# Kernel optimization log

Hardware: AMD Instinct MI355X
Metric: run time of the kernel (lower is better)

The kernel has to match this reference:

```python
import jax, jax.numpy as jnp
import numpy as np
import math

N = 100000; NFEAT = 500; M = 512; HIDDEN = 128; NLAYER = 2; K = 10; NCLASS = 40; ALPHA = 0.1


def setup_inputs() -> dict:
    key = jax.random.key(0)
    ks = jax.random.split(key, 20)
    s_in = 1.0 / math.sqrt(NFEAT); s_h = 1.0 / math.sqrt(HIDDEN); s_e = 1.0 / math.sqrt(HIDDEN + 1)
    kvec = jnp.arange(K + 1, dtype=jnp.float32)
    fW = ALPHA * (1.0 - ALPHA) ** kvec
    fW = fW.at[-1].set((1.0 - ALPHA) ** K)
    return {
        "x": jax.random.normal(ks[0], (N, NFEAT), jnp.float32),
        "e0": jax.random.uniform(ks[1], (M,), jnp.float32) * 2.0,
        "e1": jax.random.uniform(ks[2], (M,), jnp.float32) * 2.0,
        "u0": jax.random.normal(ks[3], (N, M), jnp.float32) / math.sqrt(N),
        "u1": jax.random.normal(ks[4], (N, M), jnp.float32) / math.sqrt(N),
        "fe_w1": jax.random.uniform(ks[5], (NFEAT, HIDDEN), jnp.float32, -s_in, s_in),
        "fe_b1": jnp.zeros((HIDDEN,), jnp.float32),
        "fe_w2": jax.random.uniform(ks[6], (HIDDEN, HIDDEN), jnp.float32, -s_h, s_h),
        "fe_b2": jnp.zeros((HIDDEN,), jnp.float32),
        "eig_w": jax.random.uniform(ks[7], (HIDDEN + 1, 1), jnp.float32, -s_e, s_e),
        "eig_b": jnp.zeros((1,), jnp.float32),
        "layer_weight": 0.01 * jax.random.normal(ks[8], (NLAYER, 2, HIDDEN), jnp.float32),
        "ln_gamma": jnp.ones((NLAYER, HIDDEN), jnp.float32),
        "ln_beta": jnp.zeros((NLAYER, HIDDEN), jnp.float32),
        "fW": fW,
        "att0": jax.random.uniform(ks[9], (HIDDEN, 1), jnp.float32, -1.0, 1.0),
        "att1": jax.random.uniform(ks[10], (HIDDEN, 1), jnp.float32, -1.0, 1.0),
        "att2": jax.random.uniform(ks[11], (HIDDEN, 1), jnp.float32, -1.0, 1.0),
        "att_vec": jax.random.uniform(ks[12], (3, 3), jnp.float32, -1.0 / math.sqrt(3.0), 1.0 / math.sqrt(3.0)),
        "lin3_w": jax.random.uniform(ks[13], (HIDDEN, NCLASS), jnp.float32, -s_h, s_h),
        "lin3_b": jnp.zeros((NCLASS,), jnp.float32),
    }


def _fourier_encode(e, eig_w, eig_b):
    # e: [m] -> [m, 1]; constant-1 column then cos(k*pi*e), k=1..HIDDEN
    freqs = jnp.arange(1, HIDDEN + 1, dtype=e.dtype)
    eeig = jnp.concatenate([jnp.ones((e.shape[0], 1), e.dtype),
                            jnp.cos(math.pi * e[:, None] * freqs)], axis=1)
    return eeig @ eig_w + eig_b  # [m, 1]


def _mfnn_layer(feats, w, g, b):
    # feats: [N, 2, H]; weight [2, H] -> sum over bases, LayerNorm, ReLU
    h = jnp.sum(feats * w, axis=1)
    mu = jnp.mean(h, axis=-1, keepdims=True)
    var = jnp.var(h, axis=-1, keepdims=True)
    h = (h - mu) * jax.lax.rsqrt(var + 1e-5) * g + b
    return jax.nn.relu(h)


def reference(x, e0, e1, u0, u1, fe_w1, fe_b1, fe_w2, fe_b2, eig_w, eig_b,
              layer_weight, ln_gamma, ln_beta, fW, att0, att1, att2, att_vec,
              lin3_w, lin3_b):
    h = jax.nn.relu(x @ fe_w1 + fe_b1) @ fe_w2 + fe_b2  # feat_encoder (dropouts are eval no-ops)
    result = [h]
    tail = jnp.sum(fW[1:])  # r is invariant across the K inner steps: hidden = fW[0]*h + sum(fW[1:])*r
    for e_i, u_i in ((e0, u0), (e1, u1)):
        eig = _fourier_encode(e_i, eig_w, eig_b)  # [m, 1]
        for L in range(NLAYER):
            utx = u_i.T @ h                # [m, H]
            r = u_i @ (eig * utx)          # [N, H] spectral propagation
            hidden = h * fW[0] + tail * r
            feats = jnp.stack([h, hidden], axis=1)  # [N, 2, H]
            h = _mfnn_layer(feats, layer_weight[L], ln_gamma[L], ln_beta[L])
        result.append(h)
    logits = jax.nn.sigmoid(jnp.concatenate(
        [result[0] @ att0, result[1] @ att1, result[2] @ att2], axis=1)) @ att_vec
    att = jax.nn.softmax(logits, axis=1)  # [N, 3]
    h = att[:, 0:1] * result[0] + att[:, 1:2] * result[1] + att[:, 2:3] * result[2]
    return jax.nn.log_softmax(h @ lin3_w + lin3_b, axis=1)
```

## Files before the change

kernel.cpp:

```cpp
#include <hip/hip_runtime.h>
#include <stdint.h>

#define NR 100000L
#define KC 92
#define CHN 1088L

typedef __attribute__((ext_vector_type(8))) short s16x8;
typedef __attribute__((ext_vector_type(4))) short s16x4;
typedef __attribute__((ext_vector_type(4))) float f32x4;

__device__ __forceinline__ unsigned short f2bf(float f) {
  union { float f; unsigned u; } v; v.f = f;
  unsigned r = v.u + 0x7FFFu + ((v.u >> 16) & 1u);
  return (unsigned short)(r >> 16);
}
__device__ __forceinline__ float bf2f(unsigned short s) {
  union { unsigned u; float f; } v; v.u = ((unsigned)s) << 16;
  return v.f;
}
__device__ __forceinline__ f32x4 MF(s16x8 a, s16x8 b, f32x4 c) {
  return __builtin_amdgcn_mfma_f32_16x16x32_bf16(a, b, c, 0, 0, 0);
}


__device__ __forceinline__ int swz(int row, int col) {
  return row * 64 + (((col >> 3) ^ (row & 7)) << 3) + (col & 7);
}

__device__ __forceinline__ void gld16(const void* g, void* l) {
  __builtin_amdgcn_global_load_lds(
      (const __attribute__((address_space(1))) void*)g,
      (__attribute__((address_space(3))) void*)l, 16, 0, 0);
}

template<int ROWS>
__device__ __forceinline__ void stage_async(unsigned short* lds, const unsigned short* src,
    long pitch, long r0, long k0, int tid) {
  const int lane = tid & 63, w = tid >> 6;
  const int lr = lane >> 3, lc = lane & 7;
#pragma unroll
  for (int it = 0; it < ROWS / 32; ++it) {
    const int rowbase = w * (ROWS / 4) + it * 8;
    const int row = rowbase + lr;
    const int sc = lc ^ (row & 7);
    gld16(src + (r0 + row) * pitch + k0 + sc * 8, lds + rowbase * 64);
  }
}

template<int ROWS>
__device__ __forceinline__ void stage_guard(unsigned short* lds, const unsigned short* src,
    long pitch, long r0, long rlim, long k0, long klim, int tid) {
  const int f8 = tid & 7;
#pragma unroll
  for (int it = 0; it < ROWS / 32; ++it) {
    const int row = (tid >> 3) + it * 32;
    const long gr = r0 + row, gk = k0 + f8 * 8;
    s16x8 v = {};
    if (gr < rlim && gk < klim) v = *(const s16x8*)(src + gr * pitch + gk);
    *(s16x8*)(lds + row * 64 + ((f8 ^ (row & 7)) << 3)) = v;
  }
}

template<int ROWS>
__device__ __forceinline__ void stage_guard_f32(unsigned short* lds, const float* src,
    long pitch, long r0, long rlim, long k0, long klim, int tid) {
  const int f4 = tid & 15;
#pragma unroll
  for (int it = 0; it < ROWS / 16; ++it) {
    const int row = (tid >> 4) + it * 16;
    const long gr = r0 + row, gk = k0 + f4 * 4;
    f32x4 v = {};
    if (gr < rlim && gk < klim) v = *(const f32x4*)(src + gr * pitch + gk);
    s16x4 o;
    o[0] = (short)f2bf(v[0]); o[1] = (short)f2bf(v[1]);
    o[2] = (short)f2bf(v[2]); o[3] = (short)f2bf(v[3]);
    const int c = f4 >> 1, h = f4 & 1;
    *(s16x4*)(lds + row * 64 + ((c ^ (row & 7)) << 3) + h * 4) = o;
  }
}

__device__ __forceinline__ void stage_utr_f32(unsigned short* lds, const float* u,
    long n0, long m0, int tid) {
  const int mm = tid & 63;
  const int base = tid >> 6;
#pragma unroll
  for (int it = 0; it < 16; ++it) {
    const int nl = base + it * 4;
    const long n = n0 + nl;
    unsigned short v = 0;
    if (n < NR) v = f2bf(u[n * 512 + m0 + mm]);
    lds[swz(mm, nl)] = v;
  }
}

__device__ __forceinline__ s16x8 fragA(const unsigned short* lds, int row, int kk, int lane) {
  const int c = kk * 4 + (lane >> 4);
  return *(const s16x8*)(lds + row * 64 + ((c ^ (row & 7)) << 3));
}

__global__ void k_prep(const float* __restrict__ e0, const float* __restrict__ e1,
    const float* __restrict__ fe_w1, const float* __restrict__ fe_w2,
    const float* __restrict__ eig_w, const float* __restrict__ eig_b,
    const float* __restrict__ lw, const float* __restrict__ fW,
    unsigned short* __restrict__ W1T, unsigned short* __restrict__ W2T,
    float* __restrict__ eig, float* __restrict__ coef) {
  long id = (long)blockIdx.x * 256 + threadIdx.x;
  if (id < 65536) {
    int j = (int)(id >> 9), k = (int)(id & 511);
    W1T[id] = (k < 500) ? f2bf(fe_w1[(long)k * 128 + j]) : (unsigned short)0;
  } else if (id < 65536 + 16384) {
    long q = id - 65536; int j = (int)(q >> 7), k = (int)(q & 127);
    W2T[q] = f2bf(fe_w2[(long)k * 128 + j]);
  } else if (id < 65536 + 16384 + 1024) {
    long q = id - 65536 - 16384; int b = (int)(q >> 9), m = (int)(q & 511);
    const float* e = b ? e1 : e0;
    float s = eig_b[0] + eig_w[0];
    float pe = 3.14159265358979323846f * e[m];
    for (int f = 1; f <= 128; ++f) s += cosf(pe * (float)f) * eig_w[f];
    eig[q] = s;
  } else if (id < 65536 + 16384 + 1024 + 256) {
    long q = id - 65536 - 16384 - 1024; int L = (int)(q >> 7), j = (int)(q & 127);
    float tail = 0.f;
    for (int k = 1; k <= 10; ++k) tail += fW[k];
    float w0 = lw[L * 256 + j], w1 = lw[L * 256 + 128 + j];
    coef[L * 256 + j] = w0 + fW[0] * w1;
    coef[L * 256 + 128 + j] = tail * w1;
  }
}

__global__ __launch_bounds__(256) void k_cvtx(const float* __restrict__ x,
    unsigned short* __restrict__ xb) {
  const long t = (long)blockIdx.x * 256 + threadIdx.x;
  const int k4 = (int)(t & 127) * 4;
  const long n = t >> 7;
  s16x4 o = {};
  if (k4 < 500) {
    f32x4 v = *(const f32x4*)(x + n * 500 + k4);
    o[0] = (short)f2bf(v[0]); o[1] = (short)f2bf(v[1]);
    o[2] = (short)f2bf(v[2]); o[3] = (short)f2bf(v[3]);
  }
  *(s16x4*)(xb + n * 512 + k4) = o;
}

__global__ __launch_bounds__(256) void k_cvtT(const float* __restrict__ u,
    unsigned short* __restrict__ Ubf, unsigned short* __restrict__ UbT) {
  __shared__ float T[64][68];
  const int tid = threadIdx.x;
  const int nt = blockIdx.x >> 3, mt = blockIdx.x & 7;
  const long n0 = (long)nt * 64, m0 = (long)mt * 64;
  const int c8 = (tid & 7) * 8;
  const int r = tid >> 3;
#pragma unroll
  for (int p = 0; p < 2; ++p) {
    const int rr = r + p * 32;
    const long n = n0 + rr;
    f32x4 a = {}, b = {};
    if (n < NR) {
      a = *(const f32x4*)(u + n * 512 + m0 + c8);
      b = *(const f32x4*)(u + n * 512 + m0 + c8 + 4);
    }
    *(f32x4*)&T[rr][c8] = a;
    *(f32x4*)&T[rr][c8 + 4] = b;
    if (n < NR) {
      s16x8 o;
      o[0] = (short)f2bf(a[0]); o[1] = (short)f2bf(a[1]);
      o[2] = (short)f2bf(a[2]); o[3] = (short)f2bf(a[3]);
      o[4] = (short)f2bf(b[0]); o[5] = (short)f2bf(b[1]);
      o[6] = (short)f2bf(b[2]); o[7] = (short)f2bf(b[3]);
      *(s16x8*)(Ubf + n * 512 + m0 + c8) = o;
    }
  }
  __syncthreads();
  const int nb8 = (tid & 7) * 8;
#pragma unroll
  for (int p = 0; p < 2; ++p) {
    const int mm = r + p * 32;
    s16x8 o;
#pragma unroll
    for (int e = 0; e < 8; ++e) o[e] = (short)f2bf(T[nb8 + e][mm]);
    const long nb = n0 + nb8;
    if (nb + 7 < NR) {
      *(s16x8*)(UbT + (long)(m0 + mm) * NR + nb) = o;
    } else {
#pragma unroll
      for (int e = 0; e < 8; ++e)
        if (nb + e < NR) UbT[(long)(m0 + mm) * NR + nb + e] = o[e];
    }
  }
}

__global__ __launch_bounds__(256) void k_gemm1(const unsigned short* __restrict__ xb,
    const unsigned short* __restrict__ W1T, const float* __restrict__ b1,
    unsigned short* __restrict__ t) {
  __shared__ __align__(16) unsigned short Al[128 * 64];
  __shared__ __align__(16) unsigned short Bl[128 * 64];
  const int tid = threadIdx.x, lane = tid & 63, w = tid >> 6;
  const long n0 = (long)blockIdx.x * 128;
  const bool edge = (n0 + 128) > NR;
  f32x4 acc[2][8] = {};
  for (int kt = 0; kt < 8; ++kt) {
    if (!edge) stage_async<128>(Al, xb, 512, n0, kt * 64L, tid);
    else       stage_guard<128>(Al, xb, 512, n0, NR, kt * 64L, 512, tid);
    stage_async<128>(Bl, W1T, 512, 0, kt * 64L, tid);
    __syncthreads();
#pragma unroll
    for (int kk = 0; kk < 2; ++kk) {
      s16x8 af0 = fragA(Al, w * 32 + (lane & 15), kk, lane);
      s16x8 af1 = fragA(Al, w * 32 + 16 + (lane & 15), kk, lane);
#pragma unroll
      for (int ct = 0; ct < 8; ++ct) {
        s16x8 bfr = fragA(Bl, ct * 16 + (lane & 15), kk, lane);
        acc[0][ct] = MF(af0, bfr, acc[0][ct]);
        acc[1][ct] = MF(af1, bfr, acc[1][ct]);
      }
    }
    __syncthreads();
  }
  const int cl = lane & 15, g = lane >> 4;
#pragma unroll
  for (int ct = 0; ct < 8; ++ct) {
    const int j = ct * 16 + cl;
    const float bias = b1[j];
#pragma unroll
    for (int rt = 0; rt < 2; ++rt)
#pragma unroll
      for (int r = 0; r < 4; ++r) {
        const long n = n0 + w * 32 + rt * 16 + (g << 2) + r;
        if (n < NR) {
          float v = acc[rt][ct][r] + bias;
          t[n * 128 + j] = f2bf(v > 0.f ? v : 0.f);
        }
      }
  }
}

__global__ __launch_bounds__(256) void k_gemm1f(const float* __restrict__ x,
    const unsigned short* __restrict__ W1T, const float* __restrict__ b1,
    unsigned short* __restrict__ t) {
  __shared__ __align__(16) unsigned short Al[64 * 64];
  __shared__ __align__(16) unsigned short Bl[128 * 64];
  const int tid = threadIdx.x, lane = tid & 63, w = tid >> 6;
  const long n0 = (long)blockIdx.x * 64;
  f32x4 acc[8] = {};
  for (int kt = 0; kt < 8; ++kt) {
    stage_guard_f32<64>(Al, x, 500, n0, NR, kt * 64L, 500, tid);
    stage_guard<128>(Bl, W1T, 512, 0, 1L << 40, kt * 64L, 512, tid);
    __syncthreads();
#pragma unroll
    for (int kk = 0; kk < 2; ++kk) {
      s16x8 af = fragA(Al, (w << 4) + (lane & 15), kk, lane);
#pragma unroll
      for (int ct = 0; ct < 8; ++ct) {
        s16x8 bfr = fragA(Bl, (ct << 4) + (lane & 15), kk, lane);
        acc[ct] = MF(af, bfr, acc[ct]);
      }
    }
    __syncthreads();
  }
  const int cl = lane & 15, g = lane >> 4;
#pragma unroll
  for (int ct = 0; ct < 8; ++ct) {
    int j = (ct << 4) + cl;
    float bias = b1[j];
#pragma unroll
    for (int r = 0; r < 4; ++r) {
      long n = n0 + (w << 4) + (g << 2) + r;
      if (n < NR) {
        float v = acc[ct][r] + bias;
        t[n * 128 + j] = f2bf(v > 0.f ? v : 0.f);
      }
    }
  }
}

__global__ __launch_bounds__(256) void k_gemm2(const unsigned short* __restrict__ W2T,
    const unsigned short* __restrict__ t, const float* __restrict__ b2,
    unsigned short* __restrict__ hT) {
  __shared__ __align__(16) unsigned short Al[128 * 64];
  __shared__ __align__(16) unsigned short Bl[128 * 64];
  const int tid = threadIdx.x, lane = tid & 63, w = tid >> 6;
  const long n0 = (long)blockIdx.x * 128;
  const bool edge = (n0 + 128) > NR;
  f32x4 acc[8][2] = {};
  for (int kt = 0; kt < 2; ++kt) {
    stage_async<128>(Al, W2T, 128, 0, kt * 64L, tid);
    if (!edge) stage_async<128>(Bl, t, 128, n0, kt * 64L, tid);
    else       stage_guard<128>(Bl, t, 128, n0, NR, kt * 64L, 128, tid);
    __syncthreads();
#pragma unroll
    for (int kk = 0; kk < 2; ++kk) {
      s16x8 bf0 = fragA(Bl, w * 32 + (lane & 15), kk, lane);
      s16x8 bf1 = fragA(Bl, w * 32 + 16 + (lane & 15), kk, lane);
#pragma unroll
      for (int rt = 0; rt < 8; ++rt) {
        s16x8 af = fragA(Al, rt * 16 + (lane & 15), kk, lane);
        acc[rt][0] = MF(af, bf0, acc[rt][0]);
        acc[rt][1] = MF(af, bf1, acc[rt][1]);
      }
    }
    __syncthreads();
  }
  const int cl = lane & 15, g = lane >> 4;
#pragma unroll
  for (int rt = 0; rt < 8; ++rt)
#pragma unroll
    for (int r = 0; r < 4; ++r) {
      const int j = rt * 16 + (g << 2) + r;
      const float bias = b2[j];
#pragma unroll
      for (int ct = 0; ct < 2; ++ct) {
        const long n = n0 + w * 32 + ct * 16 + cl;
        if (n < NR) hT[(long)j * NR + n] = f2bf(acc[rt][ct][r] + bias);
      }
    }
}

__global__ __launch_bounds__(256) void k_utx(const unsigned short* __restrict__ hT,
    const unsigned short* __restrict__ UbT, float* __restrict__ P) {
  __shared__ __align__(16) unsigned short Al[128 * 64];
  __shared__ __align__(16) unsigned short Bl[128 * 64];
  const int tid = threadIdx.x, lane = tid & 63, w = tid >> 6;
  const int mt = blockIdx.x & 3, c = blockIdx.x >> 2;
  const long m0 = (long)mt * 128, nb = (long)c * CHN;
  f32x4 acc[8][2] = {};
  for (int kt = 0; kt < 17; ++kt) {
    const long n0 = nb + kt * 64;
    if (n0 + 64 <= NR) {
      stage_async<128>(Al, hT, NR, 0, n0, tid);
      stage_async<128>(Bl, UbT, NR, m0, n0, tid);
    } else {
      stage_guard<128>(Al, hT, NR, 0, 1L << 40, n0, NR, tid);
      stage_guard<128>(Bl, UbT, NR, m0, 1L << 40, n0, NR, tid);
    }
    __syncthreads();
#pragma unroll
    for (int kk = 0; kk < 2; ++kk) {
      s16x8 bf0 = fragA(Bl, w * 32 + (lane & 15), kk, lane);
      s16x8 bf1 = fragA(Bl, w * 32 + 16 + (lane & 15), kk, lane);
#pragma unroll
      for (int rt = 0; rt < 8; ++rt) {
        s16x8 af = fragA(Al, rt * 16 + (lane & 15), kk, lane);
        acc[rt][0] = MF(af, bf0, acc[rt][0]);
        acc[rt][1] = MF(af, bf1, acc[rt][1]);
      }
    }
    __syncthreads();
  }
  const int cl = lane & 15, g = lane >> 4;
  float* Pc = P + (long)c * 65536;
#pragma unroll
  for (int rt = 0; rt < 8; ++rt)
#pragma unroll
    for (int r = 0; r < 4; ++r) {
      const int j = rt * 16 + (g << 2) + r;
#pragma unroll
      for (int ct = 0; ct < 2; ++ct) {
        const long m = m0 + w * 32 + ct * 16 + cl;
        Pc[(long)j * 512 + m] = acc[rt][ct][r];
      }
    }
}

__global__ __launch_bounds__(256) void k_utx0(const unsigned short* __restrict__ hT,
    const float* __restrict__ u, float* __restrict__ P) {
  __shared__ __align__(16) unsigned short Al[128 * 64];
  __shared__ __align__(16) unsigned short Bl[64 * 64];
  const int tid = threadIdx.x, lane = tid & 63, w = tid >> 6;
  const int mt = blockIdx.x & 7, c = blockIdx.x >> 3;
  const long m0 = (long)mt * 64, nb = (long)c * CHN;
  f32x4 acc[8] = {};
  for (int kt = 0; kt < 17; ++kt) {
    const long n0 = nb + kt * 64;
    stage_guard<128>(Al, hT, NR, 0, 1L << 40, n0, NR, tid);
    stage_utr_f32(Bl, u, n0, m0, tid);
    __syncthreads();
#pragma unroll
    for (int kk = 0; kk < 2; ++kk) {
      s16x8 bfr = fragA(Bl, (w << 4) + (lane & 15), kk, lane);
#pragma unroll
      for (int rt = 0; rt < 8; ++rt) {
        s16x8 af = fragA(Al, (rt << 4) + (lane & 15), kk, lane);
        acc[rt] = MF(af, bfr, acc[rt]);
      }
    }
    __syncthreads();
  }
  const int cl = lane & 15, g = lane >> 4;
  const long m = m0 + (w << 4) + cl;
  float* Pc = P + (long)c * 65536;
#pragma unroll
  for (int rt = 0; rt < 8; ++rt)
#pragma unroll
    for (int r = 0; r < 4; ++r) {
      int j = (rt << 4) + (g << 2) + r;
      Pc[(long)j * 512 + m] = acc[rt][r];
    }
}

__global__ void k_reduce(const float* __restrict__ P, const float* __restrict__ eig,
                         unsigned short* __restrict__ sT) {
  const int idx = blockIdx.x * 256 + threadIdx.x;
  const int m = idx & 511;
  float s = 0.f;
#pragma unroll 4
  for (int c = 0; c < KC; ++c) s += P[(long)c * 65536 + idx];
  sT[idx] = f2bf(s * eig[m]);
}

__global__ __launch_bounds__(256) void k_rgemm(const unsigned short* __restrict__ sT,
    const unsigned short* __restrict__ Ubf, const unsigned short* __restrict__ hin,
    unsigned short* __restrict__ hout, const float* __restrict__ c0,
    const float* __restrict__ c1, const float* __restrict__ gam,
    const float* __restrict__ bet) {
  __shared__ __align__(16) unsigned short Al[128 * 64];
  __shared__ __align__(16) unsigned short Bl[64 * 64];
  const int tid = threadIdx.x, lane = tid & 63, w = tid >> 6;
  const long n0 = (long)blockIdx.x * 64;
  const bool edge = (n0 + 64) > NR;
  f32x4 acc[8] = {};
  for (int kt = 0; kt < 8; ++kt) {
    stage_async<128>(Al, sT, 512, 0, kt * 64L, tid);
    if (!edge) stage_async<64>(Bl, Ubf, 512, n0, kt * 64L, tid);
    else       stage_guard<64>(Bl, Ubf, 512, n0, NR, kt * 64L, 512, tid);
    __syncthreads();
#pragma unroll
    for (int kk = 0; kk < 2; ++kk) {
      s16x8 bfr = fragA(Bl, (w << 4) + (lane & 15), kk, lane);
#pragma unroll
      for (int rt = 0; rt < 8; ++rt) {
        s16x8 af = fragA(Al, rt * 16 + (lane & 15), kk, lane);
        acc[rt] = MF(af, bfr, acc[rt]);
      }
    }
    __syncthreads();
  }
  if (!edge) stage_async<128>(Al, hin, NR, 0, n0, tid);
  else       stage_guard<128>(Al, hin, NR, 0, 1L << 40, n0, NR, tid);
  __syncthreads();
  const int cl = lane & 15, g = lane >> 4;
  const int nl = (w << 4) + cl;
  float sum = 0.f, ssq = 0.f;
#pragma unroll
  for (int rt = 0; rt < 8; ++rt)
#pragma unroll
    for (int r = 0; r < 4; ++r) {
      const int j = rt * 16 + (g << 2) + r;
      const float hp = bf2f(Al[swz(j, nl)]);
      const float pv = hp * c0[j] + c1[j] * acc[rt][r];
      acc[rt][r] = pv;
      sum += pv; ssq += pv * pv;
    }
  sum += __shfl_xor(sum, 16, 64); sum += __shfl_xor(sum, 32, 64);
  ssq += __shfl_xor(ssq, 16, 64); ssq += __shfl_xor(ssq, 32, 64);
  const float mu = sum * (1.f / 128.f);
  const float rs = rsqrtf(ssq * (1.f / 128.f) - mu * mu + 1e-5f);
  __syncthreads();
#pragma unroll
  for (int rt = 0; rt < 8; ++rt)
#pragma unroll
    for (int r = 0; r < 4; ++r) {
      const int j = rt * 16 + (g << 2) + r;
      float o = (acc[rt][r] - mu) * rs * gam[j] + bet[j];
      Al[swz(j, nl)] = f2bf(o > 0.f ? o : 0.f);
    }
  __syncthreads();
  const int f8 = tid & 7;
  const long gk = n0 + f8 * 8;
#pragma unroll
  for (int it = 0; it < 4; ++it) {
    const int j = (tid >> 3) + it * 32;
    const s16x8 v = *(const s16x8*)(Al + j * 64 + ((f8 ^ (j & 7)) << 3));
    if (gk + 7 < NR) {
      *(s16x8*)(hout + (long)j * NR + gk) = v;
    } else {
#pragma unroll
      for (int e = 0; e < 8; ++e)
        if (gk + e < NR) hout[(long)j * NR + gk + e] = v[e];
    }
  }
}

__global__ __launch_bounds__(256) void k_rgemm64(const unsigned short* __restrict__ sT,
    const float* __restrict__ u, const unsigned short* __restrict__ hin,
    unsigned short* __restrict__ hout, const float* __restrict__ c0,
    const float* __restrict__ c1, const float* __restrict__ gam,
    const float* __restrict__ bet) {
  __shared__ __align__(16) unsigned short Al[128 * 64];
  __shared__ __align__(16) unsigned short Bl[64 * 64];
  const int tid = threadIdx.x, lane = tid & 63, w = tid >> 6;
  const long n0 = (long)blockIdx.x * 64;
  f32x4 acc[8] = {};
  for (int kt = 0; kt < 8; ++kt) {
    stage_guard<128>(Al, sT, 512, 0, 1L << 40, kt * 64L, 512, tid);
    stage_guard_f32<64>(Bl, u, 512, n0, NR, kt * 64L, 512, tid);
    __syncthreads();
#pragma unroll
    for (int kk = 0; kk < 2; ++kk) {
      s16x8 bfr = fragA(Bl, (w << 4) + (lane & 15), kk, lane);
#pragma unroll
      for (int rt = 0; rt < 8; ++rt) {
        s16x8 af = fragA(Al, (rt << 4) + (lane & 15), kk, lane);
        acc[rt] = MF(af, bfr, acc[rt]);
      }
    }
    __syncthreads();
  }
  const int cl = lane & 15, g = lane >> 4;
  const long n = n0 + (w << 4) + cl;
  const bool valid = n < NR;
  float sum = 0.f, ssq = 0.f;
#pragma unroll
  for (int rt = 0; rt < 8; ++rt)
#pragma unroll
    for (int r = 0; r < 4; ++r) {
      int j = (rt << 4) + (g << 2) + r;
      float hp = valid ? bf2f(hin[(long)j * NR + n]) : 0.f;
      float pv = hp * c0[j] + c1[j] * acc[rt][r];
      acc[rt][r] = pv;
      sum += pv; ssq += pv * pv;
    }
  sum += __shfl_xor(sum, 16, 64); sum += __shfl_xor(sum, 32, 64);
  ssq += __shfl_xor(ssq, 16, 64); ssq += __shfl_xor(ssq, 32, 64);
  const float mu = sum * (1.f / 128.f);
  const float rs = rsqrtf(ssq * (1.f / 128.f) - mu * mu + 1e-5f);
  if (valid) {
#pragma unroll
    for (int rt = 0; rt < 8; ++rt)
#pragma unroll
      for (int r = 0; r < 4; ++r) {
        int j = (rt << 4) + (g << 2) + r;
        float o = (acc[rt][r] - mu) * rs * gam[j] + bet[j];
        hout[(long)j * NR + n] = f2bf(o > 0.f ? o : 0.f);
      }
  }
}

__global__ __launch_bounds__(256) void k_final(const unsigned short* __restrict__ R0,
    const unsigned short* __restrict__ R1, const unsigned short* __restrict__ R2,
    const float* __restrict__ att0, const float* __restrict__ att1,
    const float* __restrict__ att2, const float* __restrict__ av,
    const float* __restrict__ W, const float* __restrict__ bias,
    float* __restrict__ out) {
  __shared__ __align__(16) float Wl[128 * 40];
  __shared__ float Av[3][128];
  __shared__ float zb[256 * 41];
  const int tid = threadIdx.x;
  for (int i = tid; i < 5120; i += 256) Wl[i] = W[i];
  if (tid < 128) { Av[0][tid] = att0[tid]; Av[1][tid] = att1[tid]; Av[2][tid] = att2[tid]; }
  __syncthreads();
  const long n0 = (long)blockIdx.x * 256;
  const long n = n0 + tid;
  const long nn = n < NR ? n : NR - 1;
  float a0 = 0.f, a1 = 0.f, a2 = 0.f;
  for (int j = 0; j < 128; ++j) {
    a0 += bf2f(R0[(long)j * NR + nn]) * Av[0][j];
    a1 += bf2f(R1[(long)j * NR + nn]) * Av[1][j];
    a2 += bf2f(R2[(long)j * NR + nn]) * Av[2][j];
  }
  const float s0 = 1.f / (1.f + expf(-a0));
  const float s1 = 1.f / (1.f + expf(-a1));
  const float s2 = 1.f / (1.f + expf(-a2));
  const float l0 = s0 * av[0] + s1 * av[3] + s2 * av[6];
  const float l1 = s0 * av[1] + s1 * av[4] + s2 * av[7];
  const float l2 = s0 * av[2] + s1 * av[5] + s2 * av[8];
  const float mx = fmaxf(l0, fmaxf(l1, l2));
  const float e0v = expf(l0 - mx), e1v = expf(l1 - mx), e2v = expf(l2 - mx);
  const float inv = 1.f / (e0v + e1v + e2v);
  const float w0 = e0v * inv, w1 = e1v * inv, w2 = e2v * inv;
  float z[40];
#pragma unroll
  for (int c = 0; c < 40; ++c) z[c] = bias[c];
  for (int j = 0; j < 128; ++j) {
    const float h = w0 * bf2f(R0[(long)j * NR + nn]) + w1 * bf2f(R1[(long)j * NR + nn])
                  + w2 * bf2f(R2[(long)j * NR + nn]);
#pragma unroll
    for (int c4 = 0; c4 < 10; ++c4) {
      f32x4 wv = *(const f32x4*)(&Wl[j * 40 + c4 * 4]);
      z[c4 * 4 + 0] += h * wv[0];
      z[c4 * 4 + 1] += h * wv[1];
      z[c4 * 4 + 2] += h * wv[2];
      z[c4 * 4 + 3] += h * wv[3];
    }
  }
  float mz = z[0];
#pragma unroll
  for (int c = 1; c < 40; ++c) mz = fmaxf(mz, z[c]);
  float se = 0.f;
#pragma unroll
  for (int c = 0; c < 40; ++c) se += expf(z[c] - mz);
  const float ls = logf(se);
#pragma unroll
  for (int c = 0; c < 40; ++c) zb[tid * 41 + c] = z[c] - mz - ls;
  __syncthreads();
  long rows = NR - n0; if (rows > 256) rows = 256;
  const long cnt = rows * 40;
  for (long i = tid; i < cnt; i += 256)
    out[n0 * 40 + i] = zb[(i / 40) * 41 + (i % 40)];
}

extern "C" void kernel_launch(void* const* d_in, const int* in_sizes, int n_in,
                              void* d_out, int out_size, void* d_ws, size_t ws_size,
                              hipStream_t stream) {
  const float* x      = (const float*)d_in[0];
  const float* e0     = (const float*)d_in[1];
  const float* e1     = (const float*)d_in[2];
  const float* u0     = (const float*)d_in[3];
  const float* u1     = (const float*)d_in[4];
  const float* fe_w1  = (const float*)d_in[5];
  const float* fe_b1  = (const float*)d_in[6];
  const float* fe_w2  = (const float*)d_in[7];
  const float* fe_b2  = (const float*)d_in[8];
  const float* eig_w  = (const float*)d_in[9];
  const float* eig_bi = (const float*)d_in[10];
  const float* lw     = (const float*)d_in[11];
  const float* ln_g   = (const float*)d_in[12];
  const float* ln_b   = (const float*)d_in[13];
  const float* fW     = (const float*)d_in[14];
  const float* att0   = (const float*)d_in[15];
  const float* att1   = (const float*)d_in[16];
  const float* att2   = (const float*)d_in[17];
  const float* attv   = (const float*)d_in[18];
  const float* lin3w  = (const float*)d_in[19];
  const float* lin3b  = (const float*)d_in[20];
  float* out = (float*)d_out;

  const size_t SZ_H = (size_t)NR * 128 * 2;
  const size_t SZ_P = (size_t)KC * 65536 * 4;
  const size_t SZ_U = (size_t)NR * 512 * 2;
  const size_t SZ_X = (size_t)NR * 512 * 2;

  char* p = (char*)d_ws;
  unsigned short* R0T = (unsigned short*)p; p += SZ_H;
  unsigned short* R1T = (unsigned short*)p; p += SZ_H;
  unsigned short* R2T = (unsigned short*)p; p += SZ_H;
  float* P            = (float*)p;          p += SZ_P;
  unsigned short* W1T = (unsigned short*)p; p += 131072;
  unsigned short* W2T = (unsigned short*)p; p += 32768;
  unsigned short* sT  = (unsigned short*)p; p += 131072;
  float* eig          = (float*)p;          p += 4096;
  float* coef         = (float*)p;          p += 2048;
  const size_t base = (size_t)(p - (char*)d_ws);
  const bool full = ws_size >= base + SZ_X + 2 * SZ_U;
  unsigned short* xb  = nullptr;
  unsigned short* UbT = nullptr;
  unsigned short* Ubf = nullptr;
  if (full) {
    xb  = (unsigned short*)p; p += SZ_X;
    UbT = (unsigned short*)p; p += SZ_U;
    Ubf = (unsigned short*)p; p += SZ_U;
  }

  k_prep<<<325, 256, 0, stream>>>(e0, e1, fe_w1, fe_w2, eig_w, eig_bi, lw, fW,
                                  W1T, W2T, eig, coef);
  const int GB64  = (int)((NR + 63) / 64);
  const int GB128 = (int)((NR + 127) / 128);

  if (full) {
    k_cvtx<<<50000, 256, 0, stream>>>(x, xb);
    k_gemm1<<<GB128, 256, 0, stream>>>(xb, W1T, fe_b1, R1T);
  } else {
    k_gemm1f<<<GB64, 256, 0, stream>>>(x, W1T, fe_b1, R1T);
  }
  k_gemm2<<<GB128, 256, 0, stream>>>(W2T, R1T, fe_b2, R0T);

  for (int b = 0; b < 2; ++b) {
    const float* u = b ? u1 : u0;
    if (full) k_cvtT<<<GB64 * 8, 256, 0, stream>>>(u, Ubf, UbT);
    const unsigned short* hin = (b == 0) ? R0T : R1T;
    unsigned short* hb = b ? R2T : R1T;
    for (int L = 0; L < 2; ++L) {
      unsigned short* hout = hb;
      if (full) k_utx<<<4 * KC, 256, 0, stream>>>(hin, UbT, P);
      else      k_utx0<<<8 * KC, 256, 0, stream>>>(hin, u, P);
      k_reduce<<<256, 256, 0, stream>>>(P, eig + b * 512, sT);
      if (full)
        k_rgemm<<<GB64, 256, 0, stream>>>(sT, Ubf, hin, hout,
            coef + L * 256, coef + L * 256 + 128, ln_g + L * 128, ln_b + L * 128);
      else
        k_rgemm64<<<GB64, 256, 0, stream>>>(sT, u, hin, hout,
            coef + L * 256, coef + L * 256 + 128, ln_g + L * 128, ln_b + L * 128);
      hin = hout;
    }
  }
  k_final<<<(int)((NR + 255) / 256), 256, 0, stream>>>(R0T, R1T, R2T,
      att0, att1, att2, attv, lin3w, lin3b, out);
}
```

Measured before the change: 728.3 us.

## Double-buffer LDS staging in utx and rgemm kernels, split utx M tile

```diff
diff --git a/kernel.cpp b/kernel.cpp
--- a/kernel.cpp
+++ b/kernel.cpp
@@ -21,7 +21,6 @@
 __device__ __forceinline__ f32x4 MF(s16x8 a, s16x8 b, f32x4 c) {
   return __builtin_amdgcn_mfma_f32_16x16x32_bf16(a, b, c, 0, 0, 0);
 }
-
 
 __device__ __forceinline__ int swz(int row, int col) {
   return row * 64 + (((col >> 3) ^ (row & 7)) << 3) + (col & 7);
@@ -317,47 +316,58 @@
 
 __global__ __launch_bounds__(256) void k_utx(const unsigned short* __restrict__ hT,
     const unsigned short* __restrict__ UbT, float* __restrict__ P) {
-  __shared__ __align__(16) unsigned short Al[128 * 64];
-  __shared__ __align__(16) unsigned short Bl[128 * 64];
+  __shared__ __align__(16) unsigned short Al[2][128 * 64];
+  __shared__ __align__(16) unsigned short Bl[2][64 * 64];
   const int tid = threadIdx.x, lane = tid & 63, w = tid >> 6;
-  const int mt = blockIdx.x & 3, c = blockIdx.x >> 2;
-  const long m0 = (long)mt * 128, nb = (long)c * CHN;
-  f32x4 acc[8][2] = {};
+  const int mt = blockIdx.x & 7, c = blockIdx.x >> 3;
+  const long m0 = (long)mt * 64, nb = (long)c * CHN;
+  f32x4 acc[8] = {};
+  {
+    const long n0 = nb;
+    if (n0 + 64 <= NR) {
+      stage_async<128>(Al[0], hT, NR, 0, n0, tid);
+      stage_async<64>(Bl[0], UbT, NR, m0, n0, tid);
+    } else {
+      stage_guard<128>(Al[0], hT, NR, 0, 1L << 40, n0, NR, tid);
+      stage_guard<64>(Bl[0], UbT, NR, m0, 1L << 40, n0, NR, tid);
+    }
+  }
+  __syncthreads();
+  int cur = 0;
   for (int kt = 0; kt < 17; ++kt) {
-    const long n0 = nb + kt * 64;
-    if (n0 + 64 <= NR) {
-      stage_async<128>(Al, hT, NR, 0, n0, tid);
-      stage_async<128>(Bl, UbT, NR, m0, n0, tid);
-    } else {
-      stage_guard<128>(Al, hT, NR, 0, 1L << 40, n0, NR, tid);
-      stage_guard<128>(Bl, UbT, NR, m0, 1L << 40, n0, NR, tid);
-    }
-    __syncthreads();
+    if (kt < 16) {
+      const long n1 = nb + (kt + 1) * 64;
+      if (n1 + 64 <= NR) {
+        stage_async<128>(Al[cur ^ 1], hT, NR, 0, n1, tid);
+        stage_async<64>(Bl[cur ^ 1], UbT, NR, m0, n1, tid);
+      } else {
+        stage_guard<128>(Al[cur ^ 1], hT, NR, 0, 1L << 40, n1, NR, tid);
+        stage_guard<64>(Bl[cur ^ 1], UbT, NR, m0, 1L << 40, n1, NR, tid);
+      }
+    }
+    const unsigned short* Ac = Al[cur];
+    const unsigned short* Bc = Bl[cur];
 #pragma unroll
     for (int kk = 0; kk < 2; ++kk) {
-      s16x8 bf0 = fragA(Bl, w * 32 + (lane & 15), kk, lane);
-      s16x8 bf1 = fragA(Bl, w * 32 + 16 + (lane & 15), kk, lane);
+      s16x8 bfr = fragA(Bc, (w << 4) + (lane & 15), kk, lane);
 #pragma unroll
       for (int rt = 0; rt < 8; ++rt) {
-        s16x8 af = fragA(Al, rt * 16 + (lane & 15), kk, lane);
-        acc[rt][0] = MF(af, bf0, acc[rt][0]);
-        acc[rt][1] = MF(af, bf1, acc[rt][1]);
-      }
-    }
-    __syncthreads();
+        s16x8 af = fragA(Ac, rt * 16 + (lane & 15), kk, lane);
+        acc[rt] = MF(af, bfr, acc[rt]);
+      }
+    }
+    __syncthreads();
+    cur ^= 1;
   }
   const int cl = lane & 15, g = lane >> 4;
+  const long m = m0 + (w << 4) + cl;
   float* Pc = P + (long)c * 65536;
 #pragma unroll
   for (int rt = 0; rt < 8; ++rt)
 #pragma unroll
     for (int r = 0; r < 4; ++r) {
       const int j = rt * 16 + (g << 2) + r;
-#pragma unroll
-      for (int ct = 0; ct < 2; ++ct) {
-        const long m = m0 + w * 32 + ct * 16 + cl;
-        Pc[(long)j * 512 + m] = acc[rt][ct][r];
-      }
+      Pc[(long)j * 512 + m] = acc[rt][r];
     }
 }
 
@@ -412,30 +422,41 @@
     unsigned short* __restrict__ hout, const float* __restrict__ c0,
     const float* __restrict__ c1, const float* __restrict__ gam,
     const float* __restrict__ bet) {
-  __shared__ __align__(16) unsigned short Al[128 * 64];
-  __shared__ __align__(16) unsigned short Bl[64 * 64];
+  __shared__ __align__(16) unsigned short Al[2][128 * 64];
+  __shared__ __align__(16) unsigned short Bl[2][64 * 64];
   const int tid = threadIdx.x, lane = tid & 63, w = tid >> 6;
   const long n0 = (long)blockIdx.x * 64;
   const bool edge = (n0 + 64) > NR;
   f32x4 acc[8] = {};
+  stage_async<128>(Al[0], sT, 512, 0, 0, tid);
+  if (!edge) stage_async<64>(Bl[0], Ubf, 512, n0, 0, tid);
+  else       stage_guard<64>(Bl[0], Ubf, 512, n0, NR, 0, 512, tid);
+  __syncthreads();
+  int cur = 0;
   for (int kt = 0; kt < 8; ++kt) {
-    stage_async<128>(Al, sT, 512, 0, kt * 64L, tid);
-    if (!edge) stage_async<64>(Bl, Ubf, 512, n0, kt * 64L, tid);
-    else       stage_guard<64>(Bl, Ubf, 512, n0, NR, kt * 64L, 512, tid);
-    __syncthreads();
+    if (kt < 7) {
+      const long k1 = (kt + 1) * 64L;
+      stage_async<128>(Al[cur ^ 1], sT, 512, 0, k1, tid);
+      if (!edge) stage_async<64>(Bl[cur ^ 1], Ubf, 512, n0, k1, tid);
+      else       stage_guard<64>(Bl[cur ^ 1], Ubf, 512, n0, NR, k1, 512, tid);
+    }
+    const unsigned short* Ac = Al[cur];
+    const unsigned short* Bc = Bl[cur];
 #pragma unroll
     for (int kk = 0; kk < 2; ++kk) {
-      s16x8 bfr = fragA(Bl, (w << 4) + (lane & 15), kk, lane);
+      s16x8 bfr = fragA(Bc, (w << 4) + (lane & 15), kk, lane);
 #pragma unroll
       for (int rt = 0; rt < 8; ++rt) {
-        s16x8 af = fragA(Al, rt * 16 + (lane & 15), kk, lane);
+        s16x8 af = fragA(Ac, rt * 16 + (lane & 15), kk, lane);
         acc[rt] = MF(af, bfr, acc[rt]);
       }
     }
     __syncthreads();
-  }
-  if (!edge) stage_async<128>(Al, hin, NR, 0, n0, tid);
-  else       stage_guard<128>(Al, hin, NR, 0, 1L << 40, n0, NR, tid);
+    cur ^= 1;
+  }
+  unsigned short* H = Al[0];
+  if (!edge) stage_async<128>(H, hin, NR, 0, n0, tid);
+  else       stage_guard<128>(H, hin, NR, 0, 1L << 40, n0, NR, tid);
   __syncthreads();
   const int cl = lane & 15, g = lane >> 4;
   const int nl = (w << 4) + cl;
@@ -445,7 +466,7 @@
 #pragma unroll
     for (int r = 0; r < 4; ++r) {
       const int j = rt * 16 + (g << 2) + r;
-      const float hp = bf2f(Al[swz(j, nl)]);
+      const float hp = bf2f(H[swz(j, nl)]);
       const float pv = hp * c0[j] + c1[j] * acc[rt][r];
       acc[rt][r] = pv;
       sum += pv; ssq += pv * pv;
@@ -461,7 +482,7 @@
     for (int r = 0; r < 4; ++r) {
       const int j = rt * 16 + (g << 2) + r;
       float o = (acc[rt][r] - mu) * rs * gam[j] + bet[j];
-      Al[swz(j, nl)] = f2bf(o > 0.f ? o : 0.f);
+      H[swz(j, nl)] = f2bf(o > 0.f ? o : 0.f);
     }
   __syncthreads();
   const int f8 = tid & 7;
@@ -469,7 +490,7 @@
 #pragma unroll
   for (int it = 0; it < 4; ++it) {
     const int j = (tid >> 3) + it * 32;
-    const s16x8 v = *(const s16x8*)(Al + j * 64 + ((f8 ^ (j & 7)) << 3));
+    const s16x8 v = *(const s16x8*)(H + j * 64 + ((f8 ^ (j & 7)) << 3));
     if (gk + 7 < NR) {
       *(s16x8*)(hout + (long)j * NR + gk) = v;
     } else {
@@ -670,7 +691,7 @@
     unsigned short* hb = b ? R2T : R1T;
     for (int L = 0; L < 2; ++L) {
       unsigned short* hout = hb;
-      if (full) k_utx<<<4 * KC, 256, 0, stream>>>(hin, UbT, P);
+      if (full) k_utx<<<8 * KC, 256, 0, stream>>>(hin, UbT, P);
       else      k_utx0<<<8 * KC, 256, 0, stream>>>(hin, u, P);
       k_reduce<<<256, 256, 0, stream>>>(P, eig + b * 512, sT);
       if (full)
```

New measurement: 795.8 us. 1.09x slower.
